# Kernel tuning notes

Hardware: AMD Instinct MI355X
Metric: run time of the kernel (lower is better)

Reference implementation:

```python
import jax, jax.numpy as jnp
import numpy as np

H = 64    # n_hidden
N = 1535  # input nodes; total graph nodes Nn = N + 1
B = 32    # batch
BN_EPS = 1e-5


def _p(key, shape, scale=0.05):
    return (jax.random.normal(key, shape, dtype=jnp.float32) * scale)


def setup_inputs() -> dict:
    key = jax.random.key(0)
    ks = jax.random.split(key, 32)
    inp = {
        'input_xx': jax.random.normal(ks[0], (B, N, 8), dtype=jnp.float32),
        'input_yy': jax.random.normal(ks[1], (B, N), dtype=jnp.float32),
        'output_xx': jax.random.normal(ks[2], (B, 1, 8), dtype=jnp.float32),
        # fc1: Linear(9, H); fc2: Linear(H, H)
        'W1': _p(ks[3], (H, 9)), 'b1': _p(ks[4], (H,)),
        'W2': _p(ks[5], (H, H)), 'b2': _p(ks[6], (H,)),
        # enc_new_x: Linear(8, H)
        'Wenc': _p(ks[7], (H, 8)), 'benc': _p(ks[8], (H,)),
        # Q, K, V: Linear(H, H)
        'WQ': _p(ks[9], (H, H)), 'bQ': _p(ks[10], (H,)),
        'WK': _p(ks[11], (H, H)), 'bK': _p(ks[12], (H,)),
        'WV': _p(ks[13], (H, H)), 'bV': _p(ks[14], (H,)),
        # QK: Linear(2H, 1) split into the q-half and k-half of its weight row
        'wQKq': _p(ks[15], (H,)), 'wQKk': _p(ks[16], (H,)),
        'bQK': _p(ks[17], ()),
        # A2N: Linear(H, H)
        'WA': _p(ks[18], (H, H)), 'bA': _p(ks[19], (H,)),
        # BatchNorm1d affine params
        'gamma': jnp.ones((H,), jnp.float32), 'beta': jnp.zeros((H,), jnp.float32),
        # heads
        'Wmu': _p(ks[20], (1, H)), 'bmu': _p(ks[21], (1,)),
        'Wsig': _p(ks[22], (1, H)), 'bsig': _p(ks[23], (1,)),
    }
    return inp


def _forward(input_xx, input_yy, output_xx, W1, b1, W2, b2, Wenc, benc,
             WQ, bQ, WK, bK, WV, bV, wQKq, wQKk, bQK, WA, bA,
             gamma, beta, Wmu, bmu, Wsig, bsig):
    # encode input nodes: cat(x, y) -> fc1 -> relu -> fc2 -> relu
    x = jnp.concatenate([input_xx, input_yy[..., None]], axis=-1)  # [B,N,9]
    h = jax.nn.relu(x @ W1.T + b1)
    h = jax.nn.relu(h @ W2.T + b2)                                  # [B,N,H]
    out_enc = jax.nn.relu(output_xx[:, 0, :] @ Wenc.T + benc)       # [B,H]
    # nodes: [Nn, B, H]  (node axis first, matching the torch list of nodes)
    nodes = jnp.concatenate([jnp.transpose(h, (1, 0, 2)), out_enc[None]], axis=0)

    def communicate(nodes):
        q = nodes @ WQ.T + bQ  # [Nn,B,H]
        k = nodes @ WK.T + bK
        v = nodes @ WV.T + bV
        # QK(cat(q,k)) decomposes additively: score[i,b,j] = q[i,b].wq + k[j,b].wk + b
        sq = q @ wQKq          # [Nn,B]
        sk = k @ wQKk          # [Nn,B]
        scores = sq[:, :, None] + sk.T[None, :, :] + bQK  # [Nn,B,Nn]
        w_att = jax.nn.softmax(scores, axis=-1)
        aggre = jnp.einsum('ibj,jbh->ibh', w_att, v)      # [Nn,B,H]
        z = aggre @ WA.T + bA
        # BatchNorm1d in training mode, applied per node over the batch axis
        mu = jnp.mean(z, axis=1, keepdims=True)
        var = jnp.var(z, axis=1, keepdims=True)
        z = (z - mu) / jnp.sqrt(var + BN_EPS) * gamma + beta
        return jax.nn.relu(z)

    for _ in range(4):
        nodes = communicate(nodes)

    agg = jnp.max(nodes, axis=0)                # [B,H]
    mu_out = agg @ Wmu.T + bmu                  # [B,1]
    sig_out = (agg @ Wsig.T + bsig) ** 2 + 0.01 # [B,1]
    return mu_out, sig_out


def reference(input_xx, input_yy, output_xx, W1, b1, W2, b2, Wenc, benc,
              WQ, bQ, WK, bK, WV, bV, wQKq, wQKk, bQK, WA, bA,
              gamma, beta, Wmu, bmu, Wsig, bsig):
    return _forward(input_xx, input_yy, output_xx, W1, b1, W2, b2, Wenc, benc,
                    WQ, bQ, WK, bK, WV, bV, wQKq, wQKk, bQK, WA, bA,
                    gamma, beta, Wmu, bmu, Wsig, bsig)
```

## Files before the change

### kernel.cpp

```cpp
#include <hip/hip_runtime.h>
#include <math.h>

#define HD    64
#define NIN   1535
#define NN    1536
#define BB    32
#define BN_EPS 1e-5f
#define CH    64
#define NCH   24

#define WS_NUM 0
#define WS_DEN 2048

#define STS 68

__global__ __launch_bounds__(256) void k_main(
    const float* __restrict__ xx,
    const float* __restrict__ yy,
    const float* __restrict__ oxx,
    const float* __restrict__ W1, const float* __restrict__ b1,
    const float* __restrict__ W2, const float* __restrict__ b2,
    const float* __restrict__ Wenc, const float* __restrict__ benc,
    const float* __restrict__ WK, const float* __restrict__ wQKk,
    float* __restrict__ ws) {
  __shared__ float W1s[576];
  __shared__ float b1s[64], b2s[64], bencs[64], us[64];
  __shared__ float Wencs[512];
  __shared__ float W2Ts[64 * 65];
  __shared__ float xs[512];
  __shared__ float ys[64];
  __shared__ float h1s[4][64];
  __shared__ float h2s[64 * 64];
  __shared__ float sks[64], e_s[64], rbuf[256];

  const int t = threadIdx.x;
  const int blk = blockIdx.x;
  const int b = blk & 31;
  const int c = blk >> 5;

  for (int e = t; e < 576; e += 256) W1s[e] = W1[e];
  for (int e = t; e < 512; e += 256) Wencs[e] = Wenc[e];
  for (int e = t; e < 4096; e += 256) {
    int h = e >> 6, k = e & 63;
    W2Ts[k * 65 + h] = W2[e];
  }
  for (int e = t; e < 512; e += 256) {
    int j = e >> 3, k = e & 7;
    int r0 = c * CH + j;
    xs[e] = (r0 < NIN) ? xx[(size_t)b * (NIN * 8) + (size_t)r0 * 8 + k]
                       : oxx[b * 8 + k];
  }
  if (t < 64) {
    b1s[t] = b1[t]; b2s[t] = b2[t]; bencs[t] = benc[t];
    int r0 = c * CH + t;
    ys[t] = (r0 < NIN) ? yy[b * NIN + r0] : 0.f;
    float a = 0.f;
    #pragma unroll
    for (int h0 = 0; h0 < 64; h0++) a += wQKk[h0] * WK[h0 * 64 + t];
    us[t] = a;
  }
  __syncthreads();

  const int w = t >> 6, lane = t & 63;
  float* h1w = h1s[w];

  float w2r[64];
  #pragma unroll
  for (int k = 0; k < 64; k++) w2r[k] = W2Ts[k * 65 + lane];

  for (int rr = 0; rr < 16; rr++) {
    int j = w * 16 + rr;
    int r0 = c * CH + j;
    const float* xr = xs + j * 8;
    float h2;
    if (r0 < NIN) {
      const float* wr = W1s + lane * 9;
      float a = b1s[lane];
      a += xr[0] * wr[0] + xr[1] * wr[1] + xr[2] * wr[2] + xr[3] * wr[3];
      a += xr[4] * wr[4] + xr[5] * wr[5] + xr[6] * wr[6] + xr[7] * wr[7];
      a += ys[j] * wr[8];
      h1w[lane] = fmaxf(a, 0.f);
      float a0 = b2s[lane], a1 = 0.f;
      #pragma unroll
      for (int k = 0; k < 64; k += 4) {
        float4 hv = *(const float4*)(h1w + k);
        a0 += hv.x * w2r[k]     + hv.z * w2r[k + 2];
        a1 += hv.y * w2r[k + 1] + hv.w * w2r[k + 3];
      }
      h2 = fmaxf(a0 + a1, 0.f);
    } else {
      const float* wr = Wencs + lane * 8;
      float a = bencs[lane];
      #pragma unroll
      for (int k = 0; k < 8; k++) a += xr[k] * wr[k];
      h2 = fmaxf(a, 0.f);
    }
    h2s[j * 64 + lane] = h2;
    float p = h2 * us[lane];
    p += __shfl_down(p, 32); p += __shfl_down(p, 16); p += __shfl_down(p, 8);
    p += __shfl_down(p, 4);  p += __shfl_down(p, 2);  p += __shfl_down(p, 1);
    if (lane == 0) sks[j] = p;
  }
  __syncthreads();

  if (t < 64) {
    float e = expf(sks[t]);
    e_s[t] = e;
    float s = e;
    s += __shfl_down(s, 32); s += __shfl_down(s, 16); s += __shfl_down(s, 8);
    s += __shfl_down(s, 4);  s += __shfl_down(s, 2);  s += __shfl_down(s, 1);
    if (t == 0) atomicAdd(ws + WS_DEN + b, s);
  }
  __syncthreads();
  {
    float acc = 0.f;
    for (int j = w; j < 64; j += 4) acc += e_s[j] * h2s[j * 64 + lane];
    rbuf[t] = acc;
    __syncthreads();
    if (t < 64)
      atomicAdd(ws + WS_NUM + b * 64 + t,
                rbuf[t] + rbuf[64 + t] + rbuf[128 + t] + rbuf[192 + t]);
  }
}

__global__ __launch_bounds__(1024) void k_post(
    const float* __restrict__ ws,
    const float* __restrict__ WV, const float* __restrict__ bV,
    const float* __restrict__ WA, const float* __restrict__ bA,
    const float* __restrict__ gamma, const float* __restrict__ beta,
    const float* __restrict__ Wmu, const float* __restrict__ bmu,
    const float* __restrict__ Wsig, const float* __restrict__ bsig,
    float* __restrict__ out) {
  __shared__ float WAs[64 * 65];
  __shared__ float WVs[4096];
  __shared__ float WAVT[4096];
  __shared__ float st[32 * STS], zs[32 * STS];
  __shared__ float bAVs[64], scs[64], shs[64];
  __shared__ float gammas[64], betas[64], wmus[64], wsigs[64], bVs[64];
  const int t = threadIdx.x;

  for (int e = t; e < 4096; e += 1024) {
    int h = e >> 6, m = e & 63;
    WAs[h * 65 + m] = WA[e];
    WVs[e] = WV[e];
  }
  if (t < 64) {
    gammas[t] = gamma[t]; betas[t] = beta[t];
    wmus[t] = Wmu[t]; wsigs[t] = Wsig[t]; bVs[t] = bV[t];
  }
  __syncthreads();

  if (t >= 512) {
    int w2 = t - 512;
    int kg = w2 >> 6;
    int h  = w2 & 63;
    float acc[8];
    #pragma unroll
    for (int j = 0; j < 8; j++) acc[j] = 0.f;
    for (int m = 0; m < 64; m++) {
      float wa = WAs[h * 65 + m];
      const float4* wv = (const float4*)(WVs + m * 64 + kg * 8);
      float4 w0 = wv[0], w1 = wv[1];
      acc[0] += wa * w0.x; acc[1] += wa * w0.y; acc[2] += wa * w0.z; acc[3] += wa * w0.w;
      acc[4] += wa * w1.x; acc[5] += wa * w1.y; acc[6] += wa * w1.z; acc[7] += wa * w1.w;
    }
    #pragma unroll
    for (int j = 0; j < 8; j++) WAVT[(kg * 8 + j) * 64 + h] = acc[j];
    if (w2 < 64) {
      float a = bA[w2];
      #pragma unroll
      for (int k = 0; k < 64; k++) a += WAs[w2 * 65 + k] * bVs[k];
      bAVs[w2] = a;
    }
  } else {
    #pragma unroll
    for (int e = t; e < 2048; e += 512) {
      int b2 = e >> 6, hh = e & 63;
      st[b2 * STS + hh] = ws[WS_NUM + e] / ws[WS_DEN + b2];
    }
  }
  __syncthreads();

  const int bb = t >> 6;
  const int hg = t & 63;
  float wv_[64];
  #pragma unroll
  for (int k = 0; k < 64; k++) wv_[k] = WAVT[k * 64 + hg];
  const float bav = bAVs[hg];

  for (int r = 0; r < 4; r++) {
    float a0 = bav, a1 = bav;
    #pragma unroll
    for (int k = 0; k < 64; k += 4) {
      float4 v0 = *(const float4*)(st + bb * STS + k);
      float4 v1 = *(const float4*)(st + (bb + 16) * STS + k);
      a0 += v0.x * wv_[k] + v0.y * wv_[k + 1] + v0.z * wv_[k + 2] + v0.w * wv_[k + 3];
      a1 += v1.x * wv_[k] + v1.y * wv_[k + 1] + v1.z * wv_[k + 2] + v1.w * wv_[k + 3];
    }
    zs[bb * STS + hg] = a0;
    zs[(bb + 16) * STS + hg] = a1;
    __syncthreads();
    if (t < 64) {
      float s1 = 0.f;
      #pragma unroll
      for (int b2 = 0; b2 < BB; b2++) s1 += zs[b2 * STS + t];
      float mu = s1 * (1.0f / BB);
      float s2 = 0.f;
      #pragma unroll
      for (int b2 = 0; b2 < BB; b2++) {
        float d = zs[b2 * STS + t] - mu;
        s2 += d * d;
      }
      float inv = gammas[t] / sqrtf(s2 * (1.0f / BB) + BN_EPS);
      scs[t] = inv;
      shs[t] = betas[t] - mu * inv;
    }
    __syncthreads();
    for (int e = t; e < BB * 64; e += 1024) {
      int b2 = e >> 6, hh = e & 63;
      st[b2 * STS + hh] = fmaxf(zs[b2 * STS + hh] * scs[hh] + shs[hh], 0.f);
    }
    __syncthreads();
  }

  {
    int b2 = t >> 5, i = t & 31;
    float v0 = st[b2 * STS + i], v1 = st[b2 * STS + i + 32];
    float pm = v0 * wmus[i] + v1 * wmus[i + 32];
    float ps = v0 * wsigs[i] + v1 * wsigs[i + 32];
    pm += __shfl_down(pm, 16); ps += __shfl_down(ps, 16);
    pm += __shfl_down(pm, 8);  ps += __shfl_down(ps, 8);
    pm += __shfl_down(pm, 4);  ps += __shfl_down(ps, 4);
    pm += __shfl_down(pm, 2);  ps += __shfl_down(ps, 2);
    pm += __shfl_down(pm, 1);  ps += __shfl_down(ps, 1);
    if (i == 0) {
      float sg = ps + bsig[0];
      out[b2] = pm + bmu[0];
      out[BB + b2] = sg * sg + 0.01f;
    }
  }
}

extern "C" void kernel_launch(void* const* d_in, const int* in_sizes, int n_in,
                              void* d_out, int out_size, void* d_ws, size_t ws_size,
                              hipStream_t stream) {
  const float* xx   = (const float*)d_in[0];
  const float* yy   = (const float*)d_in[1];
  const float* oxx  = (const float*)d_in[2];
  const float* W1   = (const float*)d_in[3];
  const float* b1   = (const float*)d_in[4];
  const float* W2   = (const float*)d_in[5];
  const float* b2   = (const float*)d_in[6];
  const float* Wenc = (const float*)d_in[7];
  const float* benc = (const float*)d_in[8];
  const float* WK   = (const float*)d_in[11];
  const float* WV   = (const float*)d_in[13];
  const float* bV   = (const float*)d_in[14];
  const float* wQKk = (const float*)d_in[16];
  const float* WA   = (const float*)d_in[18];
  const float* bA   = (const float*)d_in[19];
  const float* gamma= (const float*)d_in[20];
  const float* beta = (const float*)d_in[21];
  const float* Wmu  = (const float*)d_in[22];
  const float* bmu  = (const float*)d_in[23];
  const float* Wsig = (const float*)d_in[24];
  const float* bsig = (const float*)d_in[25];

  float* ws  = (float*)d_ws;
  float* out = (float*)d_out;

  hipMemsetAsync(d_ws, 0, 2080 * sizeof(float), stream);

  k_main<<<BB * NCH, 256, 0, stream>>>(xx, yy, oxx, W1, b1, W2, b2, Wenc, benc,
                                       WK, wQKk, ws);
  k_post<<<1, 1024, 0, stream>>>(ws, WV, bV, WA, bA, gamma, beta,
                                 Wmu, bmu, Wsig, bsig, out);
}
```

Measured before the change: 140.0 us.

## Replace global atomics with per-chunk partial writes and drop workspace memset

Each main-kernel block now writes its partial softmax numerator and denominator to its own workspace slot instead of atomically accumulating into shared per-batch slots. The post kernel sums the 24 chunk partials itself, so the hipMemsetAsync before launch is no longer needed. The exp is also moved into the per-row reduction, which removes one shared buffer and one barrier. This removes atomic contention and a separate memset launch, at the cost of a larger workspace and more reduction work in the single-block post kernel.

```diff
diff --git a/kernel.cpp b/kernel.cpp
--- a/kernel.cpp
+++ b/kernel.cpp
@@ -9,8 +9,8 @@
 #define CH    64
 #define NCH   24
 
-#define WS_NUM 0
-#define WS_DEN 2048
+#define WS_DEN 0
+#define WS_NUM 768
 
 #define STS 68
 
@@ -31,12 +31,13 @@
   __shared__ float ys[64];
   __shared__ float h1s[4][64];
   __shared__ float h2s[64 * 64];
-  __shared__ float sks[64], e_s[64], rbuf[256];
+  __shared__ float e_s[64], rbuf[256];
 
   const int t = threadIdx.x;
   const int blk = blockIdx.x;
   const int b = blk & 31;
   const int c = blk >> 5;
+  const int pp = b * NCH + c;
 
   for (int e = t; e < 576; e += 256) W1s[e] = W1[e];
   for (int e = t; e < 512; e += 256) Wencs[e] = Wenc[e];
@@ -99,27 +100,24 @@
     float p = h2 * us[lane];
     p += __shfl_down(p, 32); p += __shfl_down(p, 16); p += __shfl_down(p, 8);
     p += __shfl_down(p, 4);  p += __shfl_down(p, 2);  p += __shfl_down(p, 1);
-    if (lane == 0) sks[j] = p;
+    if (lane == 0) e_s[j] = expf(p);
   }
   __syncthreads();
 
   if (t < 64) {
-    float e = expf(sks[t]);
-    e_s[t] = e;
-    float s = e;
+    float s = e_s[t];
     s += __shfl_down(s, 32); s += __shfl_down(s, 16); s += __shfl_down(s, 8);
     s += __shfl_down(s, 4);  s += __shfl_down(s, 2);  s += __shfl_down(s, 1);
-    if (t == 0) atomicAdd(ws + WS_DEN + b, s);
-  }
-  __syncthreads();
+    if (t == 0) ws[WS_DEN + pp] = s;
+  }
   {
     float acc = 0.f;
     for (int j = w; j < 64; j += 4) acc += e_s[j] * h2s[j * 64 + lane];
     rbuf[t] = acc;
     __syncthreads();
     if (t < 64)
-      atomicAdd(ws + WS_NUM + b * 64 + t,
-                rbuf[t] + rbuf[64 + t] + rbuf[128 + t] + rbuf[192 + t]);
+      ws[WS_NUM + (size_t)pp * 64 + t] =
+          rbuf[t] + rbuf[64 + t] + rbuf[128 + t] + rbuf[192 + t];
   }
 }
 
@@ -173,11 +171,21 @@
       bAVs[w2] = a;
     }
   } else {
-    #pragma unroll
-    for (int e = t; e < 2048; e += 512) {
-      int b2 = e >> 6, hh = e & 63;
-      st[b2 * STS + hh] = ws[WS_NUM + e] / ws[WS_DEN + b2];
-    }
+    int b2 = t >> 4, i = t & 15;
+    const float* dp = ws + WS_DEN + b2 * NCH;
+    float s = 0.f;
+    #pragma unroll
+    for (int cc = 0; cc < NCH; cc++) s += dp[cc];
+    float isb = 1.0f / s;
+    float a0 = 0.f, a1 = 0.f, a2 = 0.f, a3 = 0.f;
+    #pragma unroll
+    for (int cc = 0; cc < NCH; cc++) {
+      float4 v = *(const float4*)(ws + WS_NUM +
+                                  (size_t)(b2 * NCH + cc) * 64 + i * 4);
+      a0 += v.x; a1 += v.y; a2 += v.z; a3 += v.w;
+    }
+    float* sr = st + b2 * STS + i * 4;
+    sr[0] = a0 * isb; sr[1] = a1 * isb; sr[2] = a2 * isb; sr[3] = a3 * isb;
   }
   __syncthreads();
 
@@ -269,8 +277,6 @@
   float* ws  = (float*)d_ws;
   float* out = (float*)d_out;
 
-  hipMemsetAsync(d_ws, 0, 2080 * sizeof(float), stream);
-
   k_main<<<BB * NCH, 256, 0, stream>>>(xx, yy, oxx, W1, b1, W2, b2, Wenc, benc,
                                        WK, wQKk, ws);
   k_post<<<1, 1024, 0, stream>>>(ws, WV, bV, WA, bA, gamma, beta,
```

Result: no change. 137.9 us (-1.5%).
